# Kernel optimization log

Hardware: AMD Instinct MI355X
Metric: run time of the kernel (lower is better)

The kernel has to match this reference:

```python
import jax, jax.numpy as jnp
import numpy as np
import math

B, S, D, K = 512, 256, 768, 8  # num_heads = 1, head_size = D
HIST = 256  # hard-coded histogram size in the original module


def setup_inputs() -> dict:
    key = jax.random.key(0)
    ks = jax.random.split(key, 10)
    scale = 0.02
    return {
        "k_in": jax.random.normal(ks[0], (B, S, D), jnp.float32),
        "v_in": jax.random.normal(ks[1], (B, S, D), jnp.float32),
        "q_in": jax.random.normal(ks[2], (B, S, D), jnp.float32),
        "mask": jnp.ones((B, S, S), dtype=bool),
        "Wk": jax.random.normal(ks[3], (D, D), jnp.float32) * scale,
        "bk": jnp.zeros((D,), jnp.float32),
        "Wv": jax.random.normal(ks[4], (D, D), jnp.float32) * scale,
        "bv": jnp.zeros((D,), jnp.float32),
        "Wq": jax.random.normal(ks[5], (D, D), jnp.float32) * scale,
        "bq": jnp.zeros((D,), jnp.float32),
    }


def reference(k_in, v_in, q_in, mask, Wk, bk, Wv, bv, Wq, bq):
    # Linear projections (nn.Linear: x @ W.T + b). num_heads=1 so no head split.
    k = k_in @ Wk.T + bk                      # [B,S,D]
    v = v_in @ Wv.T + bv                      # [B,S,D] (dead code in original, kept for faithfulness)
    q = (q_in @ Wq.T + bq) / math.sqrt(D)     # [B,S,D]

    scores = jnp.einsum("bqd,bkd->bqk", q, k)            # [B,Sq,Sk]
    scores = jnp.where(mask, scores, -jnp.inf)
    attention = jax.nn.softmax(scores, axis=-1)           # dropout = identity (eval)

    # top-k key indices per query row
    _, idx = jax.lax.top_k(attention, K)                  # [B,Sq,K] int32

    # scatter_add histogram: result[b, idx[b,i,j], j] += 1; count[b,c] = sum_j result[b,c,j]
    # => count is simply a per-batch histogram of all Sq*K indices over [0, 256)
    flat = idx.reshape(B, S * K)
    count = jnp.zeros((B, HIST), jnp.float32).at[jnp.arange(B)[:, None], flat].add(1.0)

    _, s_indices = jax.lax.top_k(count, K)                # [B,K]
    return s_indices
```

## Files before the change

### kernel.cpp

```cpp
#include <hip/hip_runtime.h>
#include <cstdint>
#include <cstddef>

#define B_  512
#define S_  256
#define D_  768
#define K_  8
#define HB  256

#define SQRTD_F ((float)27.712812921102035)

__global__ __launch_bounds__(256) void kproj32(
    const float* __restrict__ X, const float* __restrict__ W,
    const float* __restrict__ b, float* __restrict__ P, int divq) {
  __shared__ __align__(16) float Xs[32][132];
  __shared__ __align__(16) float Ws[32][132];
  int bid = blockIdx.x;
  int mt = bid / 6, nt = bid % 6;
  int m0 = mt * 128, n0 = nt * 128;
  int tid = threadIdx.x;
  int tx = tid % 16, ty = tid / 16;
  float acc[8][8] = {};
  for (int kt = 0; kt < D_; kt += 32) {
    #pragma unroll
    for (int jj = 0; jj < 4; ++jj) {
      int v = tid + 256 * jj;
      int r = v / 8, kq = (v % 8) * 4;
      const float4 xf = *(const float4*)(X + (size_t)(m0 + r) * D_ + kt + kq);
      Xs[kq + 0][r] = xf.x; Xs[kq + 1][r] = xf.y;
      Xs[kq + 2][r] = xf.z; Xs[kq + 3][r] = xf.w;
      const float4 wf = *(const float4*)(W + (size_t)(n0 + r) * D_ + kt + kq);
      Ws[kq + 0][r] = wf.x; Ws[kq + 1][r] = wf.y;
      Ws[kq + 2][r] = wf.z; Ws[kq + 3][r] = wf.w;
    }
    __syncthreads();
    #pragma unroll 8
    for (int kk = 0; kk < 32; ++kk) {
      float xv[8], wv[8];
      *(float4*)(xv)     = *(const float4*)(&Xs[kk][ty * 8]);
      *(float4*)(xv + 4) = *(const float4*)(&Xs[kk][ty * 8 + 4]);
      *(float4*)(wv)     = *(const float4*)(&Ws[kk][tx * 8]);
      *(float4*)(wv + 4) = *(const float4*)(&Ws[kk][tx * 8 + 4]);
      #pragma unroll
      for (int i = 0; i < 8; ++i)
        #pragma unroll
        for (int j = 0; j < 8; ++j)
          acc[i][j] = fmaf(xv[i], wv[j], acc[i][j]);
    }
    __syncthreads();
  }
  #pragma unroll
  for (int i = 0; i < 8; ++i) {
    float* pp = P + (size_t)(m0 + ty * 8 + i) * D_ + n0 + tx * 8;
    #pragma unroll
    for (int j = 0; j < 8; ++j) {
      float v = acc[i][j] + b[n0 + tx * 8 + j];
      if (divq) v = v / SQRTD_F;
      pp[j] = v;
    }
  }
}

__global__ __launch_bounds__(256) void kscore32(
    const float* __restrict__ Qp, const float* __restrict__ Kp,
    int* __restrict__ count, int bBase) {
  __shared__ __align__(16) float Ts[32][33];
  __shared__ __align__(16) float Ks[32][258];
  __shared__ int hist[256];
  int lb = blockIdx.x / 8, qt = blockIdx.x % 8;
  int b = bBase + lb;
  int tid = threadIdx.x;
  hist[tid] = 0;
  int tx = tid % 32, ty = tid / 32;
  float acc[4][8] = {};
  for (int kt = 0; kt < D_; kt += 32) {
    {
      int r = tid / 8, kq = (tid % 8) * 4;
      const float4 f = *(const float4*)(Qp + (size_t)(lb * S_ + qt * 32 + r) * D_ + kt + kq);
      Ts[kq + 0][r] = f.x; Ts[kq + 1][r] = f.y;
      Ts[kq + 2][r] = f.z; Ts[kq + 3][r] = f.w;
    }
    {
      const float* kp = Kp + (size_t)(lb * S_ + tid) * D_ + kt;
      #pragma unroll
      for (int q = 0; q < 8; ++q) {
        const float4 f = *(const float4*)(kp + q * 4);
        Ks[q * 4 + 0][tid] = f.x; Ks[q * 4 + 1][tid] = f.y;
        Ks[q * 4 + 2][tid] = f.z; Ks[q * 4 + 3][tid] = f.w;
      }
    }
    __syncthreads();
    #pragma unroll 8
    for (int kk = 0; kk < 32; ++kk) {
      float tv[4], kv[8];
      #pragma unroll
      for (int i = 0; i < 4; ++i) tv[i] = Ts[kk][ty * 4 + i];
      *(float4*)(kv)     = *(const float4*)(&Ks[kk][tx * 8]);
      *(float4*)(kv + 4) = *(const float4*)(&Ks[kk][tx * 8 + 4]);
      #pragma unroll
      for (int i = 0; i < 4; ++i)
        #pragma unroll
        for (int j = 0; j < 8; ++j)
          acc[i][j] = fmaf(tv[i], kv[j], acc[i][j]);
    }
    __syncthreads();
  }
  for (int i = 0; i < 4; ++i) {
    unsigned live = 0xffu;
    #pragma unroll
    for (int it = 0; it < 8; ++it) {
      float bv = -3.4e38f; int bi = 1 << 30;
      #pragma unroll
      for (int j = 0; j < 8; ++j) {
        if ((live >> j) & 1u) {
          float v = acc[i][j]; int idx = tx * 8 + j;
          if (v > bv || (v == bv && idx < bi)) { bv = v; bi = idx; }
        }
      }
      #pragma unroll
      for (int off = 1; off < 32; off <<= 1) {
        float ov = __shfl_xor(bv, off);
        int   oi = __shfl_xor(bi, off);
        if (ov > bv || (ov == bv && oi < bi)) { bv = ov; bi = oi; }
      }
      if (tx == (bi >> 3)) live &= ~(1u << (bi & 7));
      if (tx == 0) atomicAdd(&hist[bi], 1);
    }
  }
  __syncthreads();
  if (hist[tid] > 0) atomicAdd(&count[(size_t)b * HB + tid], hist[tid]);
}

__global__ __launch_bounds__(64) void kfinal(const int* __restrict__ count, int* __restrict__ out) {
  int b = blockIdx.x;
  int lane = threadIdx.x;
  int c[4];
  #pragma unroll
  for (int j = 0; j < 4; ++j) c[j] = count[(size_t)b * HB + lane + 64 * j];
  #pragma unroll
  for (int it = 0; it < 8; ++it) {
    int bk = -0x7fffffff;
    #pragma unroll
    for (int j = 0; j < 4; ++j) {
      int idx = lane + 64 * j;
      int key = c[j] * 256 + (255 - idx);
      if (key > bk) bk = key;
    }
    #pragma unroll
    for (int off = 1; off < 64; off <<= 1) {
      int ok = __shfl_xor(bk, off);
      if (ok > bk) bk = ok;
    }
    int idx = 255 - (bk & 255);
    if (lane == (idx & 63)) c[idx >> 6] = -1;
    if (lane == 0) out[b * K_ + it] = idx;
  }
}

extern "C" void kernel_launch(void* const* d_in, const int* in_sizes, int n_in,
                              void* d_out, int out_size, void* d_ws, size_t ws_size,
                              hipStream_t stream) {
  const float* k_in = (const float*)d_in[0];
  const float* q_in = (const float*)d_in[2];
  const float* Wk   = (const float*)d_in[4];
  const float* bk   = (const float*)d_in[5];
  const float* Wq   = (const float*)d_in[8];
  const float* bq   = (const float*)d_in[9];

  char* ws = (char*)d_ws;
  int* cnt = (int*)ws;
  const size_t offQ = 524288;

  int CB = 64;
  while (CB > 1 && offQ + 2 * (size_t)CB * S_ * D_ * 4 > ws_size) CB >>= 1;
  const int nchunks = B_ / CB;
  float* Qp = (float*)(ws + offQ);
  float* Kp = Qp + (size_t)CB * S_ * D_;

  hipMemsetAsync(cnt, 0, (size_t)B_ * HB * 4, stream);

  for (int c = 0; c < nchunks; ++c) {
    const float* kc = k_in + (size_t)c * CB * S_ * D_;
    const float* qc = q_in + (size_t)c * CB * S_ * D_;
    kproj32<<<CB * 2 * 6, 256, 0, stream>>>(kc, Wk, bk, Kp, 0);
    kproj32<<<CB * 2 * 6, 256, 0, stream>>>(qc, Wq, bq, Qp, 1);
    kscore32<<<CB * 8, 256, 0, stream>>>(Qp, Kp, cnt, c * CB);
  }
  kfinal<<<B_, 64, 0, stream>>>(cnt, (int*)d_out);
}
```

Before: 5.453 ms.

## Double-buffer shared tiles and split thread fragments in projection and score GEMMs

Both the projection GEMM and the score GEMM now use double-buffered shared-memory tiles with a K step of 16. The next tile is prefetched into registers while the current one is computed, which removes one barrier per iteration and overlaps global loads with FMAs. Each thread's output fragment is also split into two interleaved halves (offset 64 or 128), with padding changed to 136/260 columns, to cut LDS bank conflicts and allow vectorized float4 stores. The top-k owner mapping in the score kernel is rewritten to match the new column layout. This costs extra registers for the prefetch buffers, which may lower occupancy.

Result: faster. 5.002 ms (-8.3%).

```diff
diff --git a/kernel.cpp b/kernel.cpp
--- a/kernel.cpp
+++ b/kernel.cpp
@@ -13,98 +13,171 @@
 __global__ __launch_bounds__(256) void kproj32(
     const float* __restrict__ X, const float* __restrict__ W,
     const float* __restrict__ b, float* __restrict__ P, int divq) {
-  __shared__ __align__(16) float Xs[32][132];
-  __shared__ __align__(16) float Ws[32][132];
+  __shared__ __align__(16) float Xs[2][16][136];
+  __shared__ __align__(16) float Ws[2][16][136];
   int bid = blockIdx.x;
   int mt = bid / 6, nt = bid % 6;
   int m0 = mt * 128, n0 = nt * 128;
   int tid = threadIdx.x;
   int tx = tid % 16, ty = tid / 16;
+  int r0 = tid / 4, q0 = (tid % 4) * 4;
+  const float* Xp0 = X + (size_t)(m0 + r0) * D_ + q0;
+  const float* Wp0 = W + (size_t)(n0 + r0) * D_ + q0;
   float acc[8][8] = {};
-  for (int kt = 0; kt < D_; kt += 32) {
-    #pragma unroll
-    for (int jj = 0; jj < 4; ++jj) {
-      int v = tid + 256 * jj;
-      int r = v / 8, kq = (v % 8) * 4;
-      const float4 xf = *(const float4*)(X + (size_t)(m0 + r) * D_ + kt + kq);
-      Xs[kq + 0][r] = xf.x; Xs[kq + 1][r] = xf.y;
-      Xs[kq + 2][r] = xf.z; Xs[kq + 3][r] = xf.w;
-      const float4 wf = *(const float4*)(W + (size_t)(n0 + r) * D_ + kt + kq);
-      Ws[kq + 0][r] = wf.x; Ws[kq + 1][r] = wf.y;
-      Ws[kq + 2][r] = wf.z; Ws[kq + 3][r] = wf.w;
-    }
+  float4 xr0, xr1, wr0, wr1;
+
+  xr0 = *(const float4*)(Xp0);
+  xr1 = *(const float4*)(Xp0 + (size_t)64 * D_);
+  wr0 = *(const float4*)(Wp0);
+  wr1 = *(const float4*)(Wp0 + (size_t)64 * D_);
+  {
+    Xs[0][q0 + 0][r0] = xr0.x; Xs[0][q0 + 1][r0] = xr0.y;
+    Xs[0][q0 + 2][r0] = xr0.z; Xs[0][q0 + 3][r0] = xr0.w;
+    Xs[0][q0 + 0][r0 + 64] = xr1.x; Xs[0][q0 + 1][r0 + 64] = xr1.y;
+    Xs[0][q0 + 2][r0 + 64] = xr1.z; Xs[0][q0 + 3][r0 + 64] = xr1.w;
+    Ws[0][q0 + 0][r0] = wr0.x; Ws[0][q0 + 1][r0] = wr0.y;
+    Ws[0][q0 + 2][r0] = wr0.z; Ws[0][q0 + 3][r0] = wr0.w;
+    Ws[0][q0 + 0][r0 + 64] = wr1.x; Ws[0][q0 + 1][r0 + 64] = wr1.y;
+    Ws[0][q0 + 2][r0 + 64] = wr1.z; Ws[0][q0 + 3][r0 + 64] = wr1.w;
+  }
+
+  for (int kt = 0; kt < D_; kt += 16) {
     __syncthreads();
-    #pragma unroll 8
-    for (int kk = 0; kk < 32; ++kk) {
+    int buf = (kt >> 4) & 1;
+    bool pre = (kt + 16) < D_;
+    if (pre) {
+      xr0 = *(const float4*)(Xp0 + kt + 16);
+      xr1 = *(const float4*)(Xp0 + (size_t)64 * D_ + kt + 16);
+      wr0 = *(const float4*)(Wp0 + kt + 16);
+      wr1 = *(const float4*)(Wp0 + (size_t)64 * D_ + kt + 16);
+    }
+    #pragma unroll
+    for (int kk = 0; kk < 16; ++kk) {
       float xv[8], wv[8];
-      *(float4*)(xv)     = *(const float4*)(&Xs[kk][ty * 8]);
-      *(float4*)(xv + 4) = *(const float4*)(&Xs[kk][ty * 8 + 4]);
-      *(float4*)(wv)     = *(const float4*)(&Ws[kk][tx * 8]);
-      *(float4*)(wv + 4) = *(const float4*)(&Ws[kk][tx * 8 + 4]);
+      *(float4*)(xv)     = *(const float4*)(&Xs[buf][kk][ty * 4]);
+      *(float4*)(xv + 4) = *(const float4*)(&Xs[buf][kk][64 + ty * 4]);
+      *(float4*)(wv)     = *(const float4*)(&Ws[buf][kk][tx * 4]);
+      *(float4*)(wv + 4) = *(const float4*)(&Ws[buf][kk][64 + tx * 4]);
       #pragma unroll
       for (int i = 0; i < 8; ++i)
         #pragma unroll
         for (int j = 0; j < 8; ++j)
           acc[i][j] = fmaf(xv[i], wv[j], acc[i][j]);
     }
-    __syncthreads();
-  }
+    if (pre) {
+      int nb = buf ^ 1;
+      Xs[nb][q0 + 0][r0] = xr0.x; Xs[nb][q0 + 1][r0] = xr0.y;
+      Xs[nb][q0 + 2][r0] = xr0.z; Xs[nb][q0 + 3][r0] = xr0.w;
+      Xs[nb][q0 + 0][r0 + 64] = xr1.x; Xs[nb][q0 + 1][r0 + 64] = xr1.y;
+      Xs[nb][q0 + 2][r0 + 64] = xr1.z; Xs[nb][q0 + 3][r0 + 64] = xr1.w;
+      Ws[nb][q0 + 0][r0] = wr0.x; Ws[nb][q0 + 1][r0] = wr0.y;
+      Ws[nb][q0 + 2][r0] = wr0.z; Ws[nb][q0 + 3][r0] = wr0.w;
+      Ws[nb][q0 + 0][r0 + 64] = wr1.x; Ws[nb][q0 + 1][r0 + 64] = wr1.y;
+      Ws[nb][q0 + 2][r0 + 64] = wr1.z; Ws[nb][q0 + 3][r0 + 64] = wr1.w;
+    }
+  }
+
   #pragma unroll
   for (int i = 0; i < 8; ++i) {
-    float* pp = P + (size_t)(m0 + ty * 8 + i) * D_ + n0 + tx * 8;
-    #pragma unroll
-    for (int j = 0; j < 8; ++j) {
-      float v = acc[i][j] + b[n0 + tx * 8 + j];
+    int row = m0 + ((i < 4) ? (ty * 4 + i) : (64 + ty * 4 + (i - 4)));
+    float* pp = P + (size_t)row * D_ + n0;
+    float4 s0, s1;
+    float* o0 = &s0.x; float* o1 = &s1.x;
+    #pragma unroll
+    for (int j = 0; j < 4; ++j) {
+      float v = acc[i][j] + b[n0 + tx * 4 + j];
       if (divq) v = v / SQRTD_F;
-      pp[j] = v;
-    }
+      o0[j] = v;
+    }
+    #pragma unroll
+    for (int j = 0; j < 4; ++j) {
+      float v = acc[i][4 + j] + b[n0 + 64 + tx * 4 + j];
+      if (divq) v = v / SQRTD_F;
+      o1[j] = v;
+    }
+    *(float4*)(pp + tx * 4)      = s0;
+    *(float4*)(pp + 64 + tx * 4) = s1;
   }
 }
 
 __global__ __launch_bounds__(256) void kscore32(
     const float* __restrict__ Qp, const float* __restrict__ Kp,
     int* __restrict__ count, int bBase) {
-  __shared__ __align__(16) float Ts[32][33];
-  __shared__ __align__(16) float Ks[32][258];
+  __shared__ __align__(16) float Ts[2][16][36];
+  __shared__ __align__(16) float Ks[2][16][260];
   __shared__ int hist[256];
   int lb = blockIdx.x / 8, qt = blockIdx.x % 8;
   int b = bBase + lb;
   int tid = threadIdx.x;
   hist[tid] = 0;
   int tx = tid % 32, ty = tid / 32;
+  int qr_ = tid / 4, qq = (tid % 4) * 4;
+  const float* Qrow = Qp + (size_t)(lb * S_ + qt * 32 + qr_) * D_ + qq;
+  const float* Krow = Kp + (size_t)(lb * S_ + tid) * D_;
   float acc[4][8] = {};
-  for (int kt = 0; kt < D_; kt += 32) {
-    {
-      int r = tid / 8, kq = (tid % 8) * 4;
-      const float4 f = *(const float4*)(Qp + (size_t)(lb * S_ + qt * 32 + r) * D_ + kt + kq);
-      Ts[kq + 0][r] = f.x; Ts[kq + 1][r] = f.y;
-      Ts[kq + 2][r] = f.z; Ts[kq + 3][r] = f.w;
-    }
-    {
-      const float* kp = Kp + (size_t)(lb * S_ + tid) * D_ + kt;
-      #pragma unroll
-      for (int q = 0; q < 8; ++q) {
-        const float4 f = *(const float4*)(kp + q * 4);
-        Ks[q * 4 + 0][tid] = f.x; Ks[q * 4 + 1][tid] = f.y;
-        Ks[q * 4 + 2][tid] = f.z; Ks[q * 4 + 3][tid] = f.w;
-      }
-    }
+  float4 qreg = {0, 0, 0, 0};
+  float4 kreg0, kreg1, kreg2, kreg3;
+
+  if (tid < 128) qreg = *(const float4*)(Qrow);
+  kreg0 = *(const float4*)(Krow);
+  kreg1 = *(const float4*)(Krow + 4);
+  kreg2 = *(const float4*)(Krow + 8);
+  kreg3 = *(const float4*)(Krow + 12);
+  if (tid < 128) {
+    Ts[0][qq + 0][qr_] = qreg.x; Ts[0][qq + 1][qr_] = qreg.y;
+    Ts[0][qq + 2][qr_] = qreg.z; Ts[0][qq + 3][qr_] = qreg.w;
+  }
+  {
+    Ks[0][ 0][tid] = kreg0.x; Ks[0][ 1][tid] = kreg0.y;
+    Ks[0][ 2][tid] = kreg0.z; Ks[0][ 3][tid] = kreg0.w;
+    Ks[0][ 4][tid] = kreg1.x; Ks[0][ 5][tid] = kreg1.y;
+    Ks[0][ 6][tid] = kreg1.z; Ks[0][ 7][tid] = kreg1.w;
+    Ks[0][ 8][tid] = kreg2.x; Ks[0][ 9][tid] = kreg2.y;
+    Ks[0][10][tid] = kreg2.z; Ks[0][11][tid] = kreg2.w;
+    Ks[0][12][tid] = kreg3.x; Ks[0][13][tid] = kreg3.y;
+    Ks[0][14][tid] = kreg3.z; Ks[0][15][tid] = kreg3.w;
+  }
+
+  for (int kt = 0; kt < D_; kt += 16) {
     __syncthreads();
-    #pragma unroll 8
-    for (int kk = 0; kk < 32; ++kk) {
+    int buf = (kt >> 4) & 1;
+    bool pre = (kt + 16) < D_;
+    if (pre) {
+      if (tid < 128) qreg = *(const float4*)(Qrow + kt + 16);
+      kreg0 = *(const float4*)(Krow + kt + 16);
+      kreg1 = *(const float4*)(Krow + kt + 20);
+      kreg2 = *(const float4*)(Krow + kt + 24);
+      kreg3 = *(const float4*)(Krow + kt + 28);
+    }
+    #pragma unroll
+    for (int kk = 0; kk < 16; ++kk) {
       float tv[4], kv[8];
-      #pragma unroll
-      for (int i = 0; i < 4; ++i) tv[i] = Ts[kk][ty * 4 + i];
-      *(float4*)(kv)     = *(const float4*)(&Ks[kk][tx * 8]);
-      *(float4*)(kv + 4) = *(const float4*)(&Ks[kk][tx * 8 + 4]);
+      *(float4*)(tv)     = *(const float4*)(&Ts[buf][kk][ty * 4]);
+      *(float4*)(kv)     = *(const float4*)(&Ks[buf][kk][tx * 4]);
+      *(float4*)(kv + 4) = *(const float4*)(&Ks[buf][kk][128 + tx * 4]);
       #pragma unroll
       for (int i = 0; i < 4; ++i)
         #pragma unroll
         for (int j = 0; j < 8; ++j)
           acc[i][j] = fmaf(tv[i], kv[j], acc[i][j]);
     }
-    __syncthreads();
-  }
+    if (pre) {
+      int nb = buf ^ 1;
+      if (tid < 128) {
+        Ts[nb][qq + 0][qr_] = qreg.x; Ts[nb][qq + 1][qr_] = qreg.y;
+        Ts[nb][qq + 2][qr_] = qreg.z; Ts[nb][qq + 3][qr_] = qreg.w;
+      }
+      Ks[nb][ 0][tid] = kreg0.x; Ks[nb][ 1][tid] = kreg0.y;
+      Ks[nb][ 2][tid] = kreg0.z; Ks[nb][ 3][tid] = kreg0.w;
+      Ks[nb][ 4][tid] = kreg1.x; Ks[nb][ 5][tid] = kreg1.y;
+      Ks[nb][ 6][tid] = kreg1.z; Ks[nb][ 7][tid] = kreg1.w;
+      Ks[nb][ 8][tid] = kreg2.x; Ks[nb][ 9][tid] = kreg2.y;
+      Ks[nb][10][tid] = kreg2.z; Ks[nb][11][tid] = kreg2.w;
+      Ks[nb][12][tid] = kreg3.x; Ks[nb][13][tid] = kreg3.y;
+      Ks[nb][14][tid] = kreg3.z; Ks[nb][15][tid] = kreg3.w;
+    }
+  }
+
   for (int i = 0; i < 4; ++i) {
     unsigned live = 0xffu;
     #pragma unroll
@@ -113,7 +186,8 @@
       #pragma unroll
       for (int j = 0; j < 8; ++j) {
         if ((live >> j) & 1u) {
-          float v = acc[i][j]; int idx = tx * 8 + j;
+          float v = acc[i][j];
+          int idx = (j < 4) ? (tx * 4 + j) : (128 + tx * 4 + (j - 4));
           if (v > bv || (v == bv && idx < bi)) { bv = v; bi = idx; }
         }
       }
@@ -123,7 +197,10 @@
         int   oi = __shfl_xor(bi, off);
         if (ov > bv || (ov == bv && oi < bi)) { bv = ov; bi = oi; }
       }
-      if (tx == (bi >> 3)) live &= ~(1u << (bi & 7));
+      int owner, jj;
+      if (bi < 128) { owner = bi >> 2; jj = bi & 3; }
+      else          { owner = (bi - 128) >> 2; jj = 4 + ((bi - 128) & 3); }
+      if (tx == owner) live &= ~(1u << jj);
       if (tx == 0) atomicAdd(&hist[bi], 1);
     }
   }
```
